# Kernel optimization log

Hardware: AMD Instinct MI355X
Metric: run time of the kernel (lower is better)

The kernel has to match this reference:

```python
import jax, jax.numpy as jnp
import numpy as np

EPS = 1e-4  # constant referenced as EPS in the original source (Performer stabilizer)
B, N, D = 4, 4096, 1024
H, M = 16, 256
DH = D // H  # 64


def _gaussian_orthogonal_random_matrix(n_rows, n_cols, rng):
    # blocks of QR-orthogonal matrices, rows scaled by norms of gaussian rows
    blocks = []
    for _ in range(n_rows // n_cols):
        q, _ = np.linalg.qr(rng.standard_normal((n_cols, n_cols)))
        blocks.append(q.T)
    rem = n_rows - (n_rows // n_cols) * n_cols
    if rem > 0:
        q, _ = np.linalg.qr(rng.standard_normal((n_cols, n_cols)))
        blocks.append(q.T[:rem])
    final = np.concatenate(blocks, axis=0)
    mult = np.linalg.norm(rng.standard_normal((n_rows, n_cols)), axis=1)
    return (mult[:, None] * final).astype(np.float32)


def setup_inputs() -> dict:
    key = jax.random.key(0)
    kq, kk, kv, kw = jax.random.split(key, 4)
    q = jax.random.normal(kq, (B, N, D), jnp.float32)
    k = jax.random.normal(kk, (B, N, D), jnp.float32)
    v = jax.random.normal(kv, (B, N, D), jnp.float32)
    W = jax.random.normal(kw, (D, D), jnp.float32) * 0.02  # to_out weight [out, in]
    b = jnp.zeros((D,), jnp.float32)
    proj = jnp.asarray(_gaussian_orthogonal_random_matrix(M, DH, np.random.default_rng(0)))
    return {"q": q, "k": k, "v": v, "W": W, "b": b, "proj": proj}


def _softmax_kernel(data, proj, is_query):
    # data: [B,H,N,Dh], proj: [M,Dh]
    dh = data.shape[-1]
    data_scale = dh ** (-0.25)
    scale = proj.shape[0] ** (-0.5)
    dp = jnp.einsum('bhnd,md->bhnm', data * data_scale, proj)  # [B,H,N,M]
    dn = (jnp.sum(data * data, axis=-1) * (0.5 * data_scale ** 2))[..., None]
    axes = (-1, -2) if is_query else (-1,)
    m = jax.lax.stop_gradient(jnp.max(dp, axis=axes, keepdims=True))
    return scale * jnp.exp(dp - dn - m + EPS)


def reference(q, k, v, W, b, proj):
    # split heads: b n (h d) -> b h n d
    def split(t):
        return t.reshape(B, N, H, DH).transpose(0, 2, 1, 3)
    qh, kh, vh = split(q), split(k), split(v)
    qp = _softmax_kernel(qh, proj, True)    # [B,H,N,M]
    kp = _softmax_kernel(kh, proj, False)   # [B,H,N,M]
    context = jnp.einsum('bhnm,bhne->bhme', kp, vh)          # [B,H,M,Dh]
    d_inv = 1.0 / jnp.einsum('bhnm,bhm->bhn', qp, kp.sum(axis=-2))
    out = jnp.einsum('bhme,bhnm,bhn->bhne', context, qp, d_inv)  # [B,H,N,Dh]
    out = out.transpose(0, 2, 1, 3).reshape(B, N, D)  # b h n d -> b n (h d)
    out = out @ W.T + b  # nn.Linear; dropout is identity at eval / p=0
    return out
```

## Files before the change

kernel.cpp:

```cpp
#include <hip/hip_runtime.h>
#include <hip/hip_bf16.h>
#include <stdint.h>

#define DATA_SCALE 0.35355339059327373f
#define DN_SCALE   0.0625f

typedef __bf16 bf16x8 __attribute__((ext_vector_type(8)));
typedef float  f32x4  __attribute__((ext_vector_type(4)));

static __device__ __forceinline__ unsigned short f2bf(float f) {
    union { __bf16 b; unsigned short u; } t;
    t.b = (__bf16)f;
    return t.u;
}

static __device__ __forceinline__ f32x4 mfma16(bf16x8 a, bf16x8 b, f32x4 c) {
    return __builtin_amdgcn_mfma_f32_16x16x32_bf16(a, b, c, 0, 0, 0);
}

static __device__ __forceinline__ void gload16(const void* g, void* lds) {
    __builtin_amdgcn_global_load_lds(
        (const __attribute__((address_space(1))) unsigned int*)g,
        (__attribute__((address_space(3))) unsigned int*)lds, 16, 0, 0);
}

union U8 { unsigned short s[8]; __bf16 b[8]; bf16x8 v; };
union P4 { __bf16 b[4]; uint2 u2; };

__global__ __launch_bounds__(256) void k_prep(const float* __restrict__ W,
                                              const float* __restrict__ proj,
                                              unsigned short* __restrict__ Wb,
                                              unsigned short* __restrict__ projs,
                                              unsigned short* __restrict__ projs_swz) {
    int i = blockIdx.x * 256 + threadIdx.x;
    if (i < 1024 * 1024) Wb[i] = f2bf(W[i]);
    if (i < 256 * 64) {
        const int row = i >> 6, col = i & 63;
        unsigned short v = f2bf(proj[i] * DATA_SCALE);
        projs[i] = v;
        projs_swz[row * 64 + (col ^ ((row & 7) << 3))] = v;
    }
}

__global__ __launch_bounds__(256) void k_ctx(const float* __restrict__ kg,
                                             const float* __restrict__ vg,
                                             const unsigned short* __restrict__ projs,
                                             const unsigned short* __restrict__ projz,
                                             float* __restrict__ ctx_part,
                                             float* __restrict__ ksum_part,
                                             int cshift, int ntiles) {
    const int bh = blockIdx.x >> cshift, chunk = blockIdx.x & ((1 << cshift) - 1);
    const int b = bh >> 4, h = bh & 15;
    const int tid = threadIdx.x;
    const int w = tid >> 6, lane = tid & 63, l15 = lane & 15, hh = lane >> 4;

    __shared__ __align__(16) unsigned short kpT[256][72];
    __shared__ __align__(16) unsigned short VT[64][72];
    __shared__ __align__(16) unsigned short pjL[256 * 64];

#pragma unroll
    for (int i = 0; i < 8; ++i) {
        const int blk = i*4 + w;
        gload16((const char*)projz + blk*1024 + lane*16, (char*)pjL + blk*1024);
    }

    bf16x8 pb0r[16];
#pragma unroll
    for (int ni = 0; ni < 16; ++ni)
        pb0r[ni] = *(const bf16x8*)(projs + (size_t)(16*ni + l15) * 64 + 8*hh);

    f32x4 cacc[4][4];
#pragma unroll
    for (int i = 0; i < 4; ++i)
#pragma unroll
        for (int j = 0; j < 4; ++j) cacc[i][j] = (f32x4){0.f, 0.f, 0.f, 0.f};
    float ksacc[16];
#pragma unroll
    for (int i = 0; i < 16; ++i) ksacc[i] = 0.f;

    const size_t rowoff = (size_t)(b * 4096 + chunk * ntiles * 64) * 1024 + h * 64;

    const float* vbase = vg + rowoff + (size_t)lane * 1024 + w * 16;
    const float* kbase = kg + rowoff + (size_t)(16*w + l15) * 1024 + hh * 8;

    float4 v0 = *(const float4*)(vbase);
    float4 v1 = *(const float4*)(vbase + 4);
    float4 v2 = *(const float4*)(vbase + 8);
    float4 v3 = *(const float4*)(vbase + 12);
    float4 k0 = *(const float4*)(kbase);
    float4 k1 = *(const float4*)(kbase + 4);
    float4 k2 = *(const float4*)(kbase + 32);
    float4 k3 = *(const float4*)(kbase + 36);

    for (int tt = 0; tt < ntiles; ++tt) {
        __syncthreads();

        {
            const int n = lane, cs = w * 16;
            VT[cs+ 0][n] = f2bf(v0.x); VT[cs+ 1][n] = f2bf(v0.y);
            VT[cs+ 2][n] = f2bf(v0.z); VT[cs+ 3][n] = f2bf(v0.w);
            VT[cs+ 4][n] = f2bf(v1.x); VT[cs+ 5][n] = f2bf(v1.y);
            VT[cs+ 6][n] = f2bf(v1.z); VT[cs+ 7][n] = f2bf(v1.w);
            VT[cs+ 8][n] = f2bf(v2.x); VT[cs+ 9][n] = f2bf(v2.y);
            VT[cs+10][n] = f2bf(v2.z); VT[cs+11][n] = f2bf(v2.w);
            VT[cs+12][n] = f2bf(v3.x); VT[cs+13][n] = f2bf(v3.y);
            VT[cs+14][n] = f2bf(v3.z); VT[cs+15][n] = f2bf(v3.w);
        }

        float s2 = k0.x*k0.x + k0.y*k0.y + k0.z*k0.z + k0.w*k0.w
                 + k1.x*k1.x + k1.y*k1.y + k1.z*k1.z + k1.w*k1.w
                 + k2.x*k2.x + k2.y*k2.y + k2.z*k2.z + k2.w*k2.w
                 + k3.x*k3.x + k3.y*k3.y + k3.z*k3.z + k3.w*k3.w;
        s2 += __shfl_xor(s2, 16);
        s2 += __shfl_xor(s2, 32);
        U8 a0, a1;
        a0.b[0]=(__bf16)k0.x; a0.b[1]=(__bf16)k0.y; a0.b[2]=(__bf16)k0.z; a0.b[3]=(__bf16)k0.w;
        a0.b[4]=(__bf16)k1.x; a0.b[5]=(__bf16)k1.y; a0.b[6]=(__bf16)k1.z; a0.b[7]=(__bf16)k1.w;
        a1.b[0]=(__bf16)k2.x; a1.b[1]=(__bf16)k2.y; a1.b[2]=(__bf16)k2.z; a1.b[3]=(__bf16)k2.w;
        a1.b[4]=(__bf16)k3.x; a1.b[5]=(__bf16)k3.y; a1.b[6]=(__bf16)k3.z; a1.b[7]=(__bf16)k3.w;

        if (tt + 1 < ntiles) {
            const float* vs = vbase + (size_t)(tt + 1) * 65536;
            v0 = *(const float4*)(vs);
            v1 = *(const float4*)(vs + 4);
            v2 = *(const float4*)(vs + 8);
            v3 = *(const float4*)(vs + 12);
            const float* ks_ = kbase + (size_t)(tt + 1) * 65536;
            k0 = *(const float4*)(ks_);
            k1 = *(const float4*)(ks_ + 4);
            k2 = *(const float4*)(ks_ + 32);
            k3 = *(const float4*)(ks_ + 36);
        }

        f32x4 sacc[16];
#pragma unroll
        for (int i = 0; i < 16; ++i) sacc[i] = (f32x4){0.f, 0.f, 0.f, 0.f};
#pragma unroll
        for (int ni = 0; ni < 16; ++ni)
            sacc[ni] = mfma16(a0.v, pb0r[ni], sacc[ni]);
#pragma unroll
        for (int ni = 0; ni < 16; ++ni) {
            bf16x8 pb1 = *(const bf16x8*)&pjL[(16*ni + l15)*64 + ((32 + 8*hh) ^ ((l15 & 7) << 3))];
            sacc[ni] = mfma16(a1.v, pb1, sacc[ni]);
        }

        float pm[4];
#pragma unroll
        for (int r = 0; r < 4; ++r) {
            float m01 = fmaxf(sacc[0][r], sacc[1][r]);
#pragma unroll
            for (int ni = 2; ni < 16; ++ni) m01 = fmaxf(m01, sacc[ni][r]);
            pm[r] = m01;
        }
#pragma unroll
        for (int msk = 1; msk <= 8; msk <<= 1)
#pragma unroll
            for (int r = 0; r < 4; ++r)
                pm[r] = fmaxf(pm[r], __shfl_xor(pm[r], msk));
        float offv[4];
#pragma unroll
        for (int r = 0; r < 4; ++r) {
            float s2r = __shfl(s2, (lane & 48) + 4*hh + r);
            offv[r] = pm[r] + DN_SCALE * s2r;
        }

#pragma unroll
        for (int ni = 0; ni < 16; ++ni) {
            float e0 = __expf(sacc[ni][0] - offv[0]);
            float e1 = __expf(sacc[ni][1] - offv[1]);
            float e2 = __expf(sacc[ni][2] - offv[2]);
            float e3 = __expf(sacc[ni][3] - offv[3]);
            ksacc[ni] += e0 + e1 + e2 + e3;
            P4 pk;
            pk.b[0]=(__bf16)e0; pk.b[1]=(__bf16)e1; pk.b[2]=(__bf16)e2; pk.b[3]=(__bf16)e3;
            const int colp = (16*w + 4*hh) ^ (8*(ni & 7));
            *(uint2*)&kpT[16*ni + l15][colp] = pk.u2;
        }
        __syncthreads();

#pragma unroll
        for (int ks = 0; ks < 2; ++ks) {
            bf16x8 am[4], bv[4];
#pragma unroll
            for (int mi = 0; mi < 4; ++mi) {
                const int row = 64*w + 16*mi + l15;
                const int s = (4*w + mi) & 7;
                am[mi] = *(const bf16x8*)&kpT[row][8*((4*ks + hh) ^ s)];
            }
#pragma unroll
            for (int ni = 0; ni < 4; ++ni)
                bv[ni] = *(const bf16x8*)&VT[16*ni + l15][ks*32 + 8*hh];
#pragma unroll
            for (int mi = 0; mi < 4; ++mi)
#pragma unroll
                for (int ni = 0; ni < 4; ++ni)
                    cacc[mi][ni] = mfma16(am[mi], bv[ni], cacc[mi][ni]);
        }
    }

#pragma unroll
    for (int ni = 0; ni < 16; ++ni) {
        ksacc[ni] += __shfl_xor(ksacc[ni], 16);
        ksacc[ni] += __shfl_xor(ksacc[ni], 32);
    }
    __syncthreads();
    float* ksW = (float*)&VT[0][0];
    if (hh == 0) {
#pragma unroll
        for (int ni = 0; ni < 16; ++ni)
            ksW[w*256 + 16*ni + l15] = ksacc[ni];
    }
    __syncthreads();
    const int pc = blockIdx.x;
    if (tid < 256)
        ksum_part[(size_t)pc * 256 + tid] = ksW[tid] + ksW[256 + tid]
                                          + ksW[512 + tid] + ksW[768 + tid];
    float* cp = ctx_part + (size_t)pc * 256 * 64;
#pragma unroll
    for (int mi = 0; mi < 4; ++mi)
#pragma unroll
        for (int ni = 0; ni < 4; ++ni)
#pragma unroll
            for (int r = 0; r < 4; ++r)
                cp[(64*w + 16*mi + 4*hh + r) * 64 + 16*ni + l15] = cacc[mi][ni][r];
}

__global__ __launch_bounds__(256) void k_reduce(const float* __restrict__ ctx_part,
                                                const float* __restrict__ ksum_part,
                                                unsigned short* __restrict__ ctxT,
                                                float* __restrict__ ksum, int nchunk) {
    const int bh = blockIdx.x >> 3, part = blockIdx.x & 7;
    const int t = threadIdx.x;
    const int m = part*32 + (t & 31);
    const int dq = t >> 5;
    const float* cp = ctx_part + (size_t)bh * nchunk * 16384 + m*64 + dq*8;
    f32x4 s[2];
#pragma unroll
    for (int j = 0; j < 2; ++j) s[j] = *(const f32x4*)(cp + j*4);
    for (int c = 1; c < nchunk; ++c) {
        const float* cc = cp + (size_t)c * 16384;
#pragma unroll
        for (int j = 0; j < 2; ++j) {
            f32x4 a = *(const f32x4*)(cc + j*4);
            s[j] += a;
        }
    }
    unsigned short* ct = ctxT + (size_t)bh * 16384;
#pragma unroll
    for (int j = 0; j < 2; ++j)
#pragma unroll
        for (int e = 0; e < 4; ++e) {
            const int dh = dq*8 + j*4 + e;
            ct[dh * 256 + (m ^ ((dh & 7) << 3))] = f2bf(s[j][e]);
        }
    if (t < 32) {
        const int m2 = part*32 + t;
        const float* kp_ = ksum_part + (size_t)bh * nchunk * 256;
        float ks = 0.f;
        for (int c = 0; c < nchunk; ++c) ks += kp_[c*256 + m2];
        ksum[(size_t)bh * 256 + m2] = ks;
    }
}

__global__ __launch_bounds__(256) void k_qout(const float* __restrict__ qg,
                                              const unsigned short* __restrict__ projs_swz,
                                              const unsigned short* __restrict__ ctxT,
                                              const float* __restrict__ ksum,
                                              unsigned short* __restrict__ attn) {
    const int lb = (blockIdx.x & 7) * 128 + (blockIdx.x >> 3);
    const int bh = lb >> 4, rg = lb & 15;
    const int b = bh >> 4, h = bh & 15;
    const int tid = threadIdx.x;
    const int w = tid >> 6, lane = tid & 63, l15 = lane & 15, hh = lane >> 4;

    __shared__ __align__(16) unsigned short pjL[256 * 64];
    __shared__ __align__(16) unsigned short ctxL[64 * 256];
    __shared__ __align__(16) unsigned short uL[4][16 * 128];

#pragma unroll
    for (int i = 0; i < 8; ++i) {
        const int blk = i*4 + w;
        gload16((const char*)projs_swz + blk*1024 + lane*16, (char*)pjL + blk*1024);
        gload16((const char*)(ctxT + (size_t)bh * 16384) + blk*1024 + lane*16,
                (char*)ctxL + blk*1024);
    }

    float ksr[16];
#pragma unroll
    for (int ni = 0; ni < 16; ++ni)
        ksr[ni] = ksum[(size_t)bh * 256 + 16*ni + l15];

    const float* qtile = qg + (size_t)(b*4096 + rg*256 + 16*w + l15) * 1024 + h*64 + hh*8;

    float4 qA[4], qB[4];
    qA[0] = *(const float4*)(qtile);
    qA[1] = *(const float4*)(qtile + 4);
    qA[2] = *(const float4*)(qtile + 32);
    qA[3] = *(const float4*)(qtile + 36);

    __syncthreads();

#pragma unroll
    for (int t = 0; t < 4; ++t) {
        const float4* qc = (t & 1) ? qB : qA;
        float4*       qn = (t & 1) ? qA : qB;

        U8 a0, a1;
        a0.b[0]=(__bf16)qc[0].x; a0.b[1]=(__bf16)qc[0].y; a0.b[2]=(__bf16)qc[0].z; a0.b[3]=(__bf16)qc[0].w;
        a0.b[4]=(__bf16)qc[1].x; a0.b[5]=(__bf16)qc[1].y; a0.b[6]=(__bf16)qc[1].z; a0.b[7]=(__bf16)qc[1].w;
        a1.b[0]=(__bf16)qc[2].x; a1.b[1]=(__bf16)qc[2].y; a1.b[2]=(__bf16)qc[2].z; a1.b[3]=(__bf16)qc[2].w;
        a1.b[4]=(__bf16)qc[3].x; a1.b[5]=(__bf16)qc[3].y; a1.b[6]=(__bf16)qc[3].z; a1.b[7]=(__bf16)qc[3].w;

        if (t < 3) {
            const float* qs = qtile + (size_t)(t + 1) * 65536;
            qn[0] = *(const float4*)(qs);
            qn[1] = *(const float4*)(qs + 4);
            qn[2] = *(const float4*)(qs + 32);
            qn[3] = *(const float4*)(qs + 36);
        }

        f32x4 sacc[16];
#pragma unroll
        for (int i = 0; i < 16; ++i) sacc[i] = (f32x4){0.f, 0.f, 0.f, 0.f};
#pragma unroll
        for (int ni = 0; ni < 16; ++ni) {
            bf16x8 pb0 = *(const bf16x8*)&pjL[(16*ni + l15)*64 + ((8*hh) ^ ((l15 & 7) << 3))];
            sacc[ni] = mfma16(a0.v, pb0, sacc[ni]);
        }
#pragma unroll
        for (int ni = 0; ni < 16; ++ni) {
            bf16x8 pb1 = *(const bf16x8*)&pjL[(16*ni + l15)*64 + ((32 + 8*hh) ^ ((l15 & 7) << 3))];
            sacc[ni] = mfma16(a1.v, pb1, sacc[ni]);
        }

        float dp[4] = {0.f, 0.f, 0.f, 0.f};
        f32x4 nacc[4];
#pragma unroll
        for (int i = 0; i < 4; ++i) nacc[i] = (f32x4){0.f, 0.f, 0.f, 0.f};

#pragma unroll
        for (int ni = 0; ni < 8; ++ni) {
#pragma unroll
            for (int r = 0; r < 4; ++r) {
                float e = __expf(sacc[ni][r]);
                dp[r] += e * ksr[ni];
                const int row = 4*hh + r;
                uL[w][row*128 + ((16*ni + l15) ^ ((row & 7) << 3))] = f2bf(e);
            }
        }
        asm volatile("s_waitcnt lgkmcnt(0)" ::: "memory");
        __builtin_amdgcn_sched_barrier(0);
#pragma unroll
        for (int ks = 0; ks < 4; ++ks) {
            bf16x8 a = *(const bf16x8*)&uL[w][l15*128 + ((ks*32 + 8*hh) ^ ((l15 & 7) << 3))];
#pragma unroll
            for (int ni = 0; ni < 4; ++ni) {
                bf16x8 bb = *(const bf16x8*)&ctxL[(16*ni + l15)*256
                                                  + ((ks*32 + 8*hh) ^ ((l15 & 7) << 3))];
                nacc[ni] = mfma16(a, bb, nacc[ni]);
            }
        }
        asm volatile("s_waitcnt lgkmcnt(0)" ::: "memory");
        __builtin_amdgcn_sched_barrier(0);

#pragma unroll
        for (int ni = 8; ni < 16; ++ni) {
#pragma unroll
            for (int r = 0; r < 4; ++r) {
                float e = __expf(sacc[ni][r]);
                dp[r] += e * ksr[ni];
                const int row = 4*hh + r;
                uL[w][row*128 + ((16*(ni-8) + l15) ^ ((row & 7) << 3))] = f2bf(e);
            }
        }
        asm volatile("s_waitcnt lgkmcnt(0)" ::: "memory");
        __builtin_amdgcn_sched_barrier(0);
#pragma unroll
        for (int ks = 4; ks < 8; ++ks) {
            bf16x8 a = *(const bf16x8*)&uL[w][l15*128 + (((ks-4)*32 + 8*hh) ^ ((l15 & 7) << 3))];
#pragma unroll
            for (int ni = 0; ni < 4; ++ni) {
                bf16x8 bb = *(const bf16x8*)&ctxL[(16*ni + l15)*256
                                                  + ((ks*32 + 8*hh) ^ ((l15 & 7) << 3))];
                nacc[ni] = mfma16(a, bb, nacc[ni]);
            }
        }

#pragma unroll
        for (int msk = 1; msk <= 8; msk <<= 1)
#pragma unroll
            for (int r = 0; r < 4; ++r)
                dp[r] += __shfl_xor(dp[r], msk);

#pragma unroll
        for (int r = 0; r < 4; ++r) {
            const float rd = 1.f / dp[r];
            const int grow = rg*256 + t*64 + 16*w + 4*hh + r;
            unsigned short* dst = attn + (size_t)(b*4096 + grow) * 1024 + h*64;
#pragma unroll
            for (int ni = 0; ni < 4; ++ni)
                dst[16*ni + l15] = f2bf(nacc[ni][r] * rd);
        }
    }
}

__global__ __launch_bounds__(256) void k_linear(const unsigned short* __restrict__ A,
                                                const unsigned short* __restrict__ Wb,
                                                const float* __restrict__ bias,
                                                float* __restrict__ out) {
    const int lb = (blockIdx.x & 7) * 128 + (blockIdx.x >> 3);
    const int bm = lb >> 3, bn = lb & 7;
    const int tid = threadIdx.x;
    const int w = tid >> 6, lane = tid & 63, l15 = lane & 15, hh = lane >> 4;
    const int wm = w >> 1, wn = w & 1;
    const int m0 = bm * 128, n0 = bn * 128;

    __shared__ __align__(16) unsigned short As[128 * 64];
    __shared__ __align__(16) unsigned short Bs[128 * 64];

    const int srow = lane >> 3;
    const int scol = (lane & 7) * 8;

    f32x4 acc[4][4];
#pragma unroll
    for (int i = 0; i < 4; ++i)
#pragma unroll
        for (int j = 0; j < 4; ++j) acc[i][j] = (f32x4){0.f, 0.f, 0.f, 0.f};

    for (int kt = 0; kt < 16; ++kt) {
        __syncthreads();
#pragma unroll
        for (int i = 0; i < 4; ++i) {
            const int rr = (w*4 + i)*8 + srow;
            gload16(A  + (size_t)(m0 + rr) * 1024 + kt*64 + scol, &As[(w*4 + i) * 512]);
            gload16(Wb + (size_t)(n0 + rr) * 1024 + kt*64 + scol, &Bs[(w*4 + i) * 512]);
        }
        __syncthreads();
#pragma unroll
        for (int ks = 0; ks < 2; ++ks) {
            bf16x8 af[4], bw[4];
#pragma unroll
            for (int mi = 0; mi < 4; ++mi)
                af[mi] = *(const bf16x8*)&As[(wm*64 + 16*mi + l15) * 64 + ks*32 + 8*hh];
#pragma unroll
            for (int ni = 0; ni < 4; ++ni)
                bw[ni] = *(const bf16x8*)&Bs[(wn*64 + 16*ni + l15) * 64 + ks*32 + 8*hh];
#pragma unroll
            for (int mi = 0; mi < 4; ++mi)
#pragma unroll
                for (int ni = 0; ni < 4; ++ni)
                    acc[mi][ni] = mfma16(af[mi], bw[ni], acc[mi][ni]);
        }
    }

    float bs[4];
#pragma unroll
    for (int ni = 0; ni < 4; ++ni) bs[ni] = bias[n0 + wn*64 + 16*ni + l15];
#pragma unroll
    for (int mi = 0; mi < 4; ++mi) {
        const int row = m0 + wm*64 + 16*mi + 4*hh;
#pragma unroll
        for (int r = 0; r < 4; ++r) {
            float* o = out + (size_t)(row + r) * 1024 + n0 + wn*64;
#pragma unroll
            for (int ni = 0; ni < 4; ++ni)
                o[16*ni + l15] = acc[mi][ni][r] + bs[ni];
        }
    }
}

extern "C" void kernel_launch(void* const* d_in, const int* in_sizes, int n_in,
                              void* d_out, int out_size, void* d_ws, size_t ws_size,
                              hipStream_t stream) {
    const float* q    = (const float*)d_in[0];
    const float* k    = (const float*)d_in[1];
    const float* v    = (const float*)d_in[2];
    const float* W    = (const float*)d_in[3];
    const float* bias = (const float*)d_in[4];
    const float* proj = (const float*)d_in[5];
    float* out = (float*)d_out;

    int nchunk = 8;
    while (nchunk > 4) {
        size_t need = 33554432ull + 2097152 + 2097152 + 65536 + 32768 + 32768
                    + (size_t)nchunk * 65536
                    + (size_t)nchunk * 4194304
                    + 4096;
        if (need <= ws_size) break;
        nchunk >>= 1;
    }
    const int cshift = (nchunk == 8) ? 3 : 2;
    const int ntiles = 64 / nchunk;

    char* ws = (char*)d_ws;
    size_t off = 0;
    unsigned short* attn  = (unsigned short*)(ws + off); off += 33554432;
    unsigned short* ctxT  = (unsigned short*)(ws + off); off += 2097152;
    unsigned short* Wb    = (unsigned short*)(ws + off); off += 2097152;
    float*          ksum  = (float*)(ws + off);          off += 65536;
    unsigned short* projs = (unsigned short*)(ws + off); off += 32768;
    unsigned short* projz = (unsigned short*)(ws + off); off += 32768;
    float*          ksump = (float*)(ws + off);          off += (size_t)nchunk * 65536;
    float*          ctxp  = (float*)(ws + off);          off += (size_t)nchunk * 4194304;

    k_prep<<<dim3(4096), dim3(256), 0, stream>>>(W, proj, Wb, projs, projz);
    k_ctx<<<dim3(64 * nchunk), dim3(256), 0, stream>>>(k, v, projs, projz, ctxp, ksump,
                                                       cshift, ntiles);
    k_reduce<<<dim3(512), dim3(256), 0, stream>>>(ctxp, ksump, ctxT, ksum, nchunk);
    k_qout<<<dim3(1024), dim3(256), 0, stream>>>(q, projz, ctxT, ksum, attn);
    k_linear<<<dim3(1024), dim3(256), 0, stream>>>(attn, Wb, bias, out);
}
```

Measured before the change: 171.0 us.

## Keep exp features in registers by transposing MFMA operands and permuting ctx layout

The q-side kernel now computes the score tile transposed (proj as A operand, q as B). Each lane's exp outputs therefore land directly in the B-operand layout for the second MFMA, which removes the per-wave LDS staging buffer, its waitcnt/sched barriers and the LDS round trip. To match, the reduce kernel writes ctxT with a permuted m index, so the register k-order lines up with the ctx columns. The row-sum uses vectorized ksum loads with fewer shuffles, and the output is written as packed 4-element stores instead of scalar bf16 stores. This relies on the permutation being exactly right, and it raises register pressure (16 packed uint2 held per lane).

Measured after the change: 172.7 us. No clear change (+1.0%).

```diff
diff --git a/kernel.cpp b/kernel.cpp
--- a/kernel.cpp
+++ b/kernel.cpp
@@ -24,7 +24,7 @@
         (__attribute__((address_space(3))) unsigned int*)lds, 16, 0, 0);
 }
 
-union U8 { unsigned short s[8]; __bf16 b[8]; bf16x8 v; };
+union U8 { unsigned short s[8]; __bf16 b[8]; unsigned int u[4]; bf16x8 v; };
 union P4 { __bf16 b[4]; uint2 u2; };
 
 __global__ __launch_bounds__(256) void k_prep(const float* __restrict__ W,
@@ -233,12 +233,14 @@
     const int t = threadIdx.x;
     const int m = part*32 + (t & 31);
     const int dq = t >> 5;
+    const int mb = m >> 4;
+    const int c = 32*(mb >> 1) + 8*((m >> 2) & 3) + 4*(mb & 1) + (m & 3);
     const float* cp = ctx_part + (size_t)bh * nchunk * 16384 + m*64 + dq*8;
     f32x4 s[2];
 #pragma unroll
     for (int j = 0; j < 2; ++j) s[j] = *(const f32x4*)(cp + j*4);
-    for (int c = 1; c < nchunk; ++c) {
-        const float* cc = cp + (size_t)c * 16384;
+    for (int cch = 1; cch < nchunk; ++cch) {
+        const float* cc = cp + (size_t)cch * 16384;
 #pragma unroll
         for (int j = 0; j < 2; ++j) {
             f32x4 a = *(const f32x4*)(cc + j*4);
@@ -251,13 +253,13 @@
 #pragma unroll
         for (int e = 0; e < 4; ++e) {
             const int dh = dq*8 + j*4 + e;
-            ct[dh * 256 + (m ^ ((dh & 7) << 3))] = f2bf(s[j][e]);
+            ct[dh * 256 + (c ^ ((dh & 7) << 3))] = f2bf(s[j][e]);
         }
     if (t < 32) {
         const int m2 = part*32 + t;
         const float* kp_ = ksum_part + (size_t)bh * nchunk * 256;
         float ks = 0.f;
-        for (int c = 0; c < nchunk; ++c) ks += kp_[c*256 + m2];
+        for (int cch = 0; cch < nchunk; ++cch) ks += kp_[cch*256 + m2];
         ksum[(size_t)bh * 256 + m2] = ks;
     }
 }
@@ -275,7 +277,6 @@
 
     __shared__ __align__(16) unsigned short pjL[256 * 64];
     __shared__ __align__(16) unsigned short ctxL[64 * 256];
-    __shared__ __align__(16) unsigned short uL[4][16 * 128];
 
 #pragma unroll
     for (int i = 0; i < 8; ++i) {
@@ -285,10 +286,10 @@
                 (char*)ctxL + blk*1024);
     }
 
-    float ksr[16];
-#pragma unroll
-    for (int ni = 0; ni < 16; ++ni)
-        ksr[ni] = ksum[(size_t)bh * 256 + 16*ni + l15];
+    f32x4 ksr4[16];
+#pragma unroll
+    for (int mb = 0; mb < 16; ++mb)
+        ksr4[mb] = *(const f32x4*)(ksum + (size_t)bh * 256 + 16*mb + 4*hh);
 
     const float* qtile = qg + (size_t)(b*4096 + rg*256 + 16*w + l15) * 1024 + h*64 + hh*8;
 
@@ -323,83 +324,60 @@
 #pragma unroll
         for (int i = 0; i < 16; ++i) sacc[i] = (f32x4){0.f, 0.f, 0.f, 0.f};
 #pragma unroll
-        for (int ni = 0; ni < 16; ++ni) {
-            bf16x8 pb0 = *(const bf16x8*)&pjL[(16*ni + l15)*64 + ((8*hh) ^ ((l15 & 7) << 3))];
-            sacc[ni] = mfma16(a0.v, pb0, sacc[ni]);
-        }
-#pragma unroll
-        for (int ni = 0; ni < 16; ++ni) {
-            bf16x8 pb1 = *(const bf16x8*)&pjL[(16*ni + l15)*64 + ((32 + 8*hh) ^ ((l15 & 7) << 3))];
-            sacc[ni] = mfma16(a1.v, pb1, sacc[ni]);
-        }
-
-        float dp[4] = {0.f, 0.f, 0.f, 0.f};
+        for (int mb = 0; mb < 16; ++mb) {
+            bf16x8 pb0 = *(const bf16x8*)&pjL[(16*mb + l15)*64 + ((8*hh) ^ ((l15 & 7) << 3))];
+            sacc[mb] = mfma16(pb0, a0.v, sacc[mb]);
+        }
+#pragma unroll
+        for (int mb = 0; mb < 16; ++mb) {
+            bf16x8 pb1 = *(const bf16x8*)&pjL[(16*mb + l15)*64 + ((32 + 8*hh) ^ ((l15 & 7) << 3))];
+            sacc[mb] = mfma16(pb1, a1.v, sacc[mb]);
+        }
+
+        float dp = 0.f;
+        uint2 p[16];
+#pragma unroll
+        for (int mb = 0; mb < 16; ++mb) {
+            float e0 = __expf(sacc[mb][0]);
+            float e1 = __expf(sacc[mb][1]);
+            float e2 = __expf(sacc[mb][2]);
+            float e3 = __expf(sacc[mb][3]);
+            dp += e0*ksr4[mb][0] + e1*ksr4[mb][1] + e2*ksr4[mb][2] + e3*ksr4[mb][3];
+            P4 pk;
+            pk.b[0]=(__bf16)e0; pk.b[1]=(__bf16)e1; pk.b[2]=(__bf16)e2; pk.b[3]=(__bf16)e3;
+            p[mb] = pk.u2;
+        }
+
         f32x4 nacc[4];
 #pragma unroll
         for (int i = 0; i < 4; ++i) nacc[i] = (f32x4){0.f, 0.f, 0.f, 0.f};
-
-#pragma unroll
-        for (int ni = 0; ni < 8; ++ni) {
-#pragma unroll
-            for (int r = 0; r < 4; ++r) {
-                float e = __expf(sacc[ni][r]);
-                dp[r] += e * ksr[ni];
-                const int row = 4*hh + r;
-                uL[w][row*128 + ((16*ni + l15) ^ ((row & 7) << 3))] = f2bf(e);
+#pragma unroll
+        for (int ks = 0; ks < 8; ++ks) {
+            U8 bf;
+            bf.u[0] = p[2*ks].x;  bf.u[1] = p[2*ks].y;
+            bf.u[2] = p[2*ks+1].x; bf.u[3] = p[2*ks+1].y;
+#pragma unroll
+            for (int mi = 0; mi < 4; ++mi) {
+                bf16x8 av = *(const bf16x8*)&ctxL[(16*mi + l15)*256
+                                                  + ((ks*32 + 8*hh) ^ ((l15 & 7) << 3))];
+                nacc[mi] = mfma16(av, bf.v, nacc[mi]);
             }
         }
-        asm volatile("s_waitcnt lgkmcnt(0)" ::: "memory");
-        __builtin_amdgcn_sched_barrier(0);
-#pragma unroll
-        for (int ks = 0; ks < 4; ++ks) {
-            bf16x8 a = *(const bf16x8*)&uL[w][l15*128 + ((ks*32 + 8*hh) ^ ((l15 & 7) << 3))];
-#pragma unroll
-            for (int ni = 0; ni < 4; ++ni) {
-                bf16x8 bb = *(const bf16x8*)&ctxL[(16*ni + l15)*256
-                                                  + ((ks*32 + 8*hh) ^ ((l15 & 7) << 3))];
-                nacc[ni] = mfma16(a, bb, nacc[ni]);
-            }
-        }
-        asm volatile("s_waitcnt lgkmcnt(0)" ::: "memory");
-        __builtin_amdgcn_sched_barrier(0);
-
-#pragma unroll
-        for (int ni = 8; ni < 16; ++ni) {
-#pragma unroll
-            for (int r = 0; r < 4; ++r) {
-                float e = __expf(sacc[ni][r]);
-                dp[r] += e * ksr[ni];
-                const int row = 4*hh + r;
-                uL[w][row*128 + ((16*(ni-8) + l15) ^ ((row & 7) << 3))] = f2bf(e);
-            }
-        }
-        asm volatile("s_waitcnt lgkmcnt(0)" ::: "memory");
-        __builtin_amdgcn_sched_barrier(0);
-#pragma unroll
-        for (int ks = 4; ks < 8; ++ks) {
-            bf16x8 a = *(const bf16x8*)&uL[w][l15*128 + (((ks-4)*32 + 8*hh) ^ ((l15 & 7) << 3))];
-#pragma unroll
-            for (int ni = 0; ni < 4; ++ni) {
-                bf16x8 bb = *(const bf16x8*)&ctxL[(16*ni + l15)*256
-                                                  + ((ks*32 + 8*hh) ^ ((l15 & 7) << 3))];
-                nacc[ni] = mfma16(a, bb, nacc[ni]);
-            }
-        }
-
-#pragma unroll
-        for (int msk = 1; msk <= 8; msk <<= 1)
-#pragma unroll
-            for (int r = 0; r < 4; ++r)
-                dp[r] += __shfl_xor(dp[r], msk);
-
-#pragma unroll
-        for (int r = 0; r < 4; ++r) {
-            const float rd = 1.f / dp[r];
-            const int grow = rg*256 + t*64 + 16*w + 4*hh + r;
-            unsigned short* dst = attn + (size_t)(b*4096 + grow) * 1024 + h*64;
-#pragma unroll
-            for (int ni = 0; ni < 4; ++ni)
-                dst[16*ni + l15] = f2bf(nacc[ni][r] * rd);
+
+        dp += __shfl_xor(dp, 16);
+        dp += __shfl_xor(dp, 32);
+        const float rd = 1.f / dp;
+
+        const int grow = rg*256 + t*64 + 16*w + l15;
+        unsigned short* dst = attn + (size_t)(b*4096 + grow) * 1024 + h*64 + 4*hh;
+#pragma unroll
+        for (int mi = 0; mi < 4; ++mi) {
+            P4 o;
+            o.b[0] = (__bf16)(nacc[mi][0] * rd);
+            o.b[1] = (__bf16)(nacc[mi][1] * rd);
+            o.b[2] = (__bf16)(nacc[mi][2] * rd);
+            o.b[3] = (__bf16)(nacc[mi][3] * rd);
+            *(uint2*)(dst + 16*mi) = o.u2;
         }
     }
 }
```
